# Optimization experiments

Hardware: AMD Instinct MI355X
Metric: run time of the kernel (lower is better)

## Reference

```python
import jax, jax.numpy as jnp
import numpy as np

B, N, DIM = 4, 1024, 1024
H, DH, ORDER = 16, 64, 3
MAXREL = 64
INNER = H * DH
VOCAB = 2 * MAXREL + 1
SCALE = DH ** -0.5
TOPK = int(0.25 * N)  # topk_ratio=0.25 default when top_k is None


def setup_inputs() -> dict:
    key = jax.random.key(0)
    ks = jax.random.split(key, 8)
    s = 0.02
    return {
        "x": jax.random.normal(ks[0], (B, N, DIM), jnp.float32),
        "Wqkv": jax.random.normal(ks[1], (3 * INNER, DIM), jnp.float32) * s,
        "bqkv": jnp.zeros((3 * INNER,), jnp.float32),
        "Wout": jax.random.normal(ks[2], (DIM, INNER), jnp.float32) * s,
        "bout": jnp.zeros((DIM,), jnp.float32),
        "rel_k_emb": jax.random.normal(ks[3], (VOCAB, DH), jnp.float32) * s,
        "rel_v_emb": jax.random.normal(ks[4], (VOCAB, DH), jnp.float32) * s,
        "alphas_raw": jax.random.normal(ks[5], (ORDER, H), jnp.float32) * 0.5,
    }


def reference(x, Wqkv, bqkv, Wout, bout, rel_k_emb, rel_v_emb, alphas_raw):
    b, n, _ = x.shape
    qkv = x @ Wqkv.T + bqkv  # [b, n, 3*inner]
    q, k, v = jnp.split(qkv, 3, axis=-1)
    to_heads = lambda t: t.reshape(b, n, H, DH).transpose(0, 2, 1, 3)  # b h n d
    q, k, v = to_heads(q), to_heads(k), to_heads(v)

    scores = jnp.einsum('bhid,bhjd->bhij', q, k) * SCALE

    # relative position bias on keys
    coords = jnp.arange(n)
    dist = jnp.clip(coords[:, None] - coords[None, :], -MAXREL, MAXREL) + MAXREL  # [n, n]
    rel_k = rel_k_emb[dist]  # [n, n, d]
    scores = scores + jnp.einsum('bhid,ijd->bhij', q, rel_k)

    # top-k thresholding per query row
    top_vals = jax.lax.top_k(scores, TOPK)[0]
    threshold = top_vals[..., -1:]
    scores = jnp.where(scores < threshold, -jnp.inf, scores)

    attn = jax.nn.softmax(scores, axis=-1)  # [b, h, n, n]

    rel_v = rel_v_emb[dist]  # [n, n, d]
    alphas = jax.nn.sigmoid(alphas_raw)  # [order, h]

    # monomial-basis polynomial filter: res = sum_i alpha_i * A^(i+1) V (+ relV term at i=0)
    res = jnp.zeros_like(v)
    v_curr = v
    for i in range(ORDER):
        a_v = jnp.einsum('bhij,bhjd->bhid', attn, v_curr)
        if i == 0:
            a_v = a_v + jnp.einsum('bhij,ijd->bhid', attn, rel_v)
        v_curr = a_v
        res = res + alphas[i][None, :, None, None] * v_curr

    out = res.transpose(0, 2, 1, 3).reshape(b, n, INNER)
    return out @ Wout.T + bout
```

## Files before the change

### kernel.cpp

```cpp
#include <hip/hip_runtime.h>

typedef unsigned short u16;
typedef unsigned int   u32;
typedef unsigned long long u64;
typedef __bf16 bf16x8 __attribute__((ext_vector_type(8)));
typedef float  floatx4 __attribute__((ext_vector_type(4)));

#define DEV static __device__ __forceinline__

DEV u16 f2bf(float f){ u32 x = __float_as_uint(f); return (u16)((x + 0x7fffu + ((x>>16)&1u)) >> 16); }
DEV float bf2f(u16 h){ return __uint_as_float(((u32)h)<<16); }
DEV u32 cvt_pk_bf16(float a, float b){ u32 r; asm("v_cvt_pk_bf16_f32 %0, %1, %2" : "=v"(r) : "v"(a), "v"(b)); return r; }

DEV void load_lds16(const u16* g, u16* l){
  __builtin_amdgcn_global_load_lds((const __attribute__((address_space(1))) u32*)g,
                                   (__attribute__((address_space(3))) u32*)l, 16, 0, 0);
}

DEV void barrier_fenced(){
  asm volatile("" ::: "memory");
  __builtin_amdgcn_sched_barrier(0);
  __builtin_amdgcn_s_barrier();
  __builtin_amdgcn_sched_barrier(0);
  asm volatile("" ::: "memory");
}

DEV u32 unswz64(u32 p){
  u32 r0 = ((p>>6) ^ (p>>8)) & 1u;
  u32 b4 = ((p>>4) & 1u) ^ r0;
  u32 b5 = ((p>>5) ^ (p>>7)) & 1u;
  return (p & ~0x70u) | (b4<<4) | (b5<<5) | (r0<<6);
}
DEV bf16x8 ldfrag(const u16* base, int row, int lane){
  u32 off = ((u32)row<<6) + (((u32)lane>>4)<<4);
  off ^= (u32)(row&7)<<4;
  return *(const bf16x8*)((const char*)base + off);
}

template<int BM, int BN>
__global__ __launch_bounds__(512, 4) void gemm8(
    const u16* __restrict__ A, const u16* __restrict__ Bm, float* __restrict__ C,
    const float* __restrict__ bias, int K, int lda, int ldb, int ldc, int ncmax)
{
  constexpr int MT = (BM/2)/16;
  constexpr int NT = (BN/4)/16;
  __shared__ u16 As[BM*32];
  __shared__ u16 Bs[BN*32];

  const int tid = threadIdx.x, wid = tid>>6, lane = tid&63;
  const int m0 = blockIdx.y * BM, n0 = blockIdx.x * BN;

  const u32 g = unswz64((u32)tid*16);
  const int srow = g>>6, schunk = (g&63)>>1;
  const u16* ga0 = A  + (long long)(m0 + srow)*lda + schunk;
  const u16* gb0 = Bm + (long long)(n0 + srow)*ldb + schunk;

  u16* lA = As + (wid<<9);
  u16* lB = Bs + (wid<<9);

  const int wm = wid>>2, wn = wid&3;
  const int lr = lane&15, lq = lane>>4;

  floatx4 acc[MT][NT] = {};

  for (int k = 0; k < K; k += 32) {
    __syncthreads();
    if (BM == 128 || wid < 4) load_lds16(ga0 + k, lA);
    load_lds16(gb0 + k, lB);
    __syncthreads();
    bf16x8 af[MT];
#pragma unroll
    for (int mt=0; mt<MT; ++mt)
      af[mt] = ldfrag(As, wm*(BM/2) + mt*16 + lr, lane);
#pragma unroll
    for (int nt=0; nt<NT; ++nt) {
      bf16x8 bfr = ldfrag(Bs, wn*(BN/4) + nt*16 + lr, lane);
#pragma unroll
      for (int mt=0; mt<MT; ++mt)
        acc[mt][nt] = __builtin_amdgcn_mfma_f32_16x16x32_bf16(af[mt], bfr, acc[mt][nt], 0, 0, 0);
    }
  }

#pragma unroll
  for (int nt=0; nt<NT; ++nt) {
    const int col = n0 + wn*(BN/4) + nt*16 + lr;
    if (col < ncmax) {
      const float bv = bias ? bias[col] : 0.f;
#pragma unroll
      for (int mt=0; mt<MT; ++mt) {
#pragma unroll
        for (int r=0; r<4; ++r) {
          const int row = m0 + wm*(BM/2) + mt*16 + lq*4 + r;
          C[(long long)row*ldc + col] = acc[mt][nt][r] + bv;
        }
      }
    }
  }
}

__global__ __launch_bounds__(512, 4) void av8(
    const u16* __restrict__ P,
    const u16* __restrict__ V,
    u16* __restrict__ vout,
    float* __restrict__ resb,
    const float* __restrict__ araw, int K, int order, int accum, int wv)
{
  __shared__ u16 smem[32768];
  const int tid = threadIdx.x, wid = tid>>6, lane = tid&63;
  const int L = blockIdx.x;
  const int z  = (L & 7) + ((L >> 7) << 3);
  const int m0 = ((L >> 3) & 15) * 64;
  const int lr = lane&15, lq = lane>>4;

  const int sw = wid & 3;
  const u32 g = unswz64((u32)(sw*1024 + lane*16));
  const int srow = g>>6, schunk = (g&63)>>1;
  const u16* gsrc = (wid < 4)
      ? P + (long long)z*1212416 + (long long)(m0 + srow)*1184 + schunk
      : V + (long long)z*75776   + (long long)srow*1184 + schunk;
  const int bsel = (wid < 4) ? 0 : 2048;
  u16* ldst0 = smem + bsel + (sw<<9);

  const int wm = wid>>2, wn = wid&3;
  const int wm32 = wm*32, wn16 = wn*16;
  const int nk = K >> 5;

  auto stage = [&](int p){ load_lds16(gsrc + (p<<5), ldst0 + ((p&7)<<12)); };

  floatx4 acc[2] = {};

#define AV_STEP(CC, VC) do { \
    asm volatile("s_waitcnt vmcnt(" VC ")" ::: "memory"); \
    barrier_fenced(); \
    const u16* Asc = smem + ((u32)(CC)<<12); \
    const u16* Bsc = Asc + 2048; \
    bf16x8 bfr = ldfrag(Bsc, wn16 + lr, lane); \
    bf16x8 af0 = ldfrag(Asc, wm32 + lr, lane); \
    bf16x8 af1 = ldfrag(Asc, wm32 + 16 + lr, lane); \
    acc[0] = __builtin_amdgcn_mfma_f32_16x16x32_bf16(af0, bfr, acc[0], 0, 0, 0); \
    acc[1] = __builtin_amdgcn_mfma_f32_16x16x32_bf16(af1, bfr, acc[1], 0, 0, 0); \
    barrier_fenced(); \
  } while(0)

#pragma unroll
  for (int p = 0; p < 8; ++p) stage(p);

  for (int s = 0; s < nk - 8; ++s){
    AV_STEP(s & 7, "7");
    stage(s + 8);
  }
  AV_STEP((nk-8) & 7, "7");
  AV_STEP((nk-7) & 7, "6");
  AV_STEP((nk-6) & 7, "5");
  AV_STEP((nk-5) & 7, "4");
  AV_STEP((nk-4) & 7, "3");
  AV_STEP((nk-3) & 7, "2");
  AV_STEP((nk-2) & 7, "1");
  AV_STEP((nk-1) & 7, "0");
#undef AV_STEP

  const int h = z & 15;
  const float alpha = 1.f/(1.f + __expf(-araw[order*16 + h]));
  float* rb = resb + (long long)z * 65536;
  const int d = wn16 + lr;
  __syncthreads();
#pragma unroll
  for (int mt=0; mt<2; ++mt){
#pragma unroll
    for (int r=0; r<4; ++r){
      const int row = wm32 + mt*16 + lq*4 + r;
      const float v = acc[mt][r];
      const long long ri = (long long)(m0+row)*64 + d;
      rb[ri] = accum ? (rb[ri] + alpha*v) : (alpha*v);
      smem[d*136 + row] = f2bf(v);
    }
  }
  __syncthreads();
  if (wv){
    const int dd = tid>>3, cc = (tid&7)*8;
    u16* vp = vout + (long long)z*75776 + (long long)dd*1184 + m0 + cc;
    const u16* sp = smem + dd*136 + cc;
    uint4 uu;
    uu.x = sp[0] | ((u32)sp[1]<<16);
    uu.y = sp[2] | ((u32)sp[3]<<16);
    uu.z = sp[4] | ((u32)sp[5]<<16);
    uu.w = sp[6] | ((u32)sp[7]<<16);
    *(uint4*)(vp) = uu;
  }
}

__global__ __launch_bounds__(1024, 8) void score_topk(
    const u16* __restrict__ qF,
    const u16* __restrict__ kxF,
    u16* __restrict__ P)
{
  constexpr int SROW = 1156;
  __shared__ float sm[16*SROW];
  const int tid = threadIdx.x, wid = tid>>6, lane = tid&63;
  const int L = blockIdx.x;
  const int z  = (L & 7) + ((L >> 9) << 3);
  const int mt = (L >> 3) & 63;
  const int m0 = mt*16;
  const int lr = lane&15, lq = lane>>4;

  const u16* Aq = qF + (((long long)z*64 + mt)*6*64 + lane)*8;
  const u16* Bq = kxF + ((long long)z*80*6*64 + lane)*8;

  bf16x8 af[6];
#pragma unroll
  for (int kc=0;kc<6;++kc) af[kc] = *(const bf16x8*)(Aq + kc*512);

  const int base = wid*5;
  {
    floatx4 acc[5];
#pragma unroll
    for (int t=0;t<5;++t) acc[t] = floatx4{0.f,0.f,0.f,0.f};
#pragma unroll
    for (int t=0;t<5;++t){
      if (base + t < 73){
        const u16* bp = Bq + (long long)(base+t)*3072;
        bf16x8 b0 = *(const bf16x8*)(bp);
        bf16x8 b1 = *(const bf16x8*)(bp + 512);
        bf16x8 b2 = *(const bf16x8*)(bp + 1024);
        bf16x8 b3 = *(const bf16x8*)(bp + 1536);
        bf16x8 b4 = *(const bf16x8*)(bp + 2048);
        bf16x8 b5 = *(const bf16x8*)(bp + 2560);
        acc[t] = __builtin_amdgcn_mfma_f32_16x16x32_bf16(af[0], b0, acc[t], 0, 0, 0);
        acc[t] = __builtin_amdgcn_mfma_f32_16x16x32_bf16(af[1], b1, acc[t], 0, 0, 0);
        acc[t] = __builtin_amdgcn_mfma_f32_16x16x32_bf16(af[2], b2, acc[t], 0, 0, 0);
        acc[t] = __builtin_amdgcn_mfma_f32_16x16x32_bf16(af[3], b3, acc[t], 0, 0, 0);
        acc[t] = __builtin_amdgcn_mfma_f32_16x16x32_bf16(af[4], b4, acc[t], 0, 0, 0);
        acc[t] = __builtin_amdgcn_mfma_f32_16x16x32_bf16(af[5], b5, acc[t], 0, 0, 0);
      }
    }
#pragma unroll
    for (int t=0;t<5;++t){
      if (base + t < 73){
        const int col = (base+t)*16 + lr;
        if (col < 1153){
#pragma unroll
          for (int r=0;r<4;++r) sm[(lq*4+r)*SROW + col] = acc[t][r];
        }
      }
    }
  }
  __syncthreads();

  {
    const int row = wid;
    const int i = m0 + row;
    float* R = sm + row*SROW;

    float v[16];
#pragma unroll
    for (int x=0;x<8;++x){
      float2 f = *(const float2*)(R + x*128 + lane*2);
      v[2*x] = f.x; v[2*x+1] = f.y;
    }
#pragma unroll
    for (int x=0;x<16;++x){
      const int j = (x>>1)*128 + lane*2 + (x&1);
      int dl = i - j; dl = dl > 64 ? 64 : (dl < -64 ? -64 : dl);
      v[x] += R[1024 + dl + 64];
    }
    u32 u[16];
#pragma unroll
    for (int x=0;x<16;++x){
      u32 bb = __float_as_uint(v[x]);
      u[x] = bb ^ ((u32)((int)bb >> 31) | 0x80000000u);
    }
    u32 thr = 0;
#pragma unroll 1
    for (int bit=31; bit>=0; --bit){
      const u32 cand = thr | (1u<<bit);
      int c = 0;
#pragma unroll
      for (int x=0;x<16;++x) c += __popcll(__ballot(u[x] >= cand));
      if (c == 256){
        u32 mn = 0xFFFFFFFFu;
#pragma unroll
        for (int x=0;x<16;++x) if (u[x] >= cand && u[x] < mn) mn = u[x];
        for (int o=32;o;o>>=1){ u32 t = __shfl_xor(mn, o); mn = t < mn ? t : mn; }
        thr = mn;
        break;
      }
      if (c > 256) thr = cand;
    }
    float m = -3.0e38f;
#pragma unroll
    for (int x=0;x<16;++x) m = fmaxf(m, v[x]);
    for (int o=32;o;o>>=1) m = fmaxf(m, __shfl_xor(m, o));
    float e[16]; float Z = 0.f;
#pragma unroll
    for (int x=0;x<16;++x){
      e[x] = (u[x] >= thr) ? __expf(v[x]-m) : 0.f;
      Z += e[x];
    }
    for (int o=32;o;o>>=1) Z += __shfl_xor(Z, o);
    const float rz = 1.f / Z;

    u16* Pr = P + ((long long)z*1024 + i)*1184;
    u32* Pr32 = (u32*)Pr;
    float s0 = 0.f, s1 = 0.f;
#pragma unroll
    for (int x=0;x<8;++x){
      const float p0 = e[2*x]*rz, p1 = e[2*x+1]*rz;
      *(float2*)(R + x*128 + lane*2) = float2{p0, p1};
      Pr32[x*64 + lane] = cvt_pk_bf16(p0, p1);
      const int j0 = x*128 + lane*2;
      if (j0     >= i+64) s0 += p0;
      if (j0     <= i-64) s1 += p0;
      if (j0 + 1 >= i+64) s0 += p1;
      if (j0 + 1 <= i-64) s1 += p1;
    }
    for (int o=32;o;o>>=1){ s0 += __shfl_xor(s0,o); s1 += __shfl_xor(s1,o); }
    {
      const int t = lane + 1;
      const int j = i + 64 - t;
      const float wv = (j>=0 && j<1024) ? R[j] : 0.f;
      Pr[1024 + t] = f2bf(wv);
      if (lane < 63){
        const int t2 = lane + 65;
        const int j2 = i + 64 - t2;
        const float wv2 = (j2>=0 && j2<1024) ? R[j2] : 0.f;
        Pr[1024 + t2] = f2bf(wv2);
      }
      if (lane == 0){ Pr[1024] = f2bf(s0); Pr[1152] = f2bf(s1); }
      if (lane >= 33) Pr[1120 + lane] = 0;
    }
  }
}

__global__ __launch_bounds__(256) void planeize(const float* __restrict__ src, u16* __restrict__ dst,
                                                int total, int modeB){
  int idx = blockIdx.x*256 + threadIdx.x;
  if (idx >= total) return;
  int c = idx & 1023, r = idx >> 10;
  float v = src[idx];
  u16 hi = f2bf(v); u16 lo = f2bf(v - bf2f(hi));
  u16* d = dst + (long long)r*3072 + c;
  if (modeB){ d[0]=hi; d[1024]=hi; d[2048]=lo; }
  else      { d[0]=hi; d[1024]=lo; d[2048]=hi; }
}

__global__ __launch_bounds__(256) void build_qk(const float* __restrict__ qkv,
                                                u16* __restrict__ qF, u16* __restrict__ kxF){
  int idx = blockIdx.x*256 + threadIdx.x;
  int d = idx & 63, n = (idx>>6) & 1023, bh = idx >> 16;
  int b = bh >> 4, h = bh & 15;
  long long src = (long long)(b*1024 + n)*3072 + h*64 + d;
  float qv = qkv[src];
  float kv = qkv[src + 1024] * 0.125f;
  u16 qhi=f2bf(qv), qlo=f2bf(qv - bf2f(qhi));
  u16 khi=f2bf(kv), klo=f2bf(kv - bf2f(khi));
  const int lane = (n&15) + (((d&31)>>3)<<4);
  const int elem = d&7, kc0 = d>>5;
  u16* q = qF + ((((long long)bh*64 + (n>>4))*6*64) + lane)*8 + elem;
  q[(kc0+0)*512] = qhi; q[(kc0+2)*512] = qlo; q[(kc0+4)*512] = qhi;
  u16* kx = kxF + ((((long long)bh*80 + (n>>4))*6*64) + lane)*8 + elem;
  kx[(kc0+0)*512] = khi; kx[(kc0+2)*512] = khi; kx[(kc0+4)*512] = klo;
}

__global__ __launch_bounds__(256) void build_kxrel(const float* __restrict__ relk, u16* __restrict__ kxF){
  int idx = blockIdx.x*256 + threadIdx.x;
  int d = idx & 63, t = (idx>>6) & 255, bh = idx >> 14;
  u16 hi=0, lo=0;
  if (t < 129){ float v = relk[t*64 + d]; hi = f2bf(v); lo = f2bf(v - bf2f(hi)); }
  const int nrow = 1024 + t;
  const int lane = (t&15) + (((d&31)>>3)<<4);
  const int elem = d&7, kc0 = d>>5;
  u16* kx = kxF + ((((long long)bh*80 + (nrow>>4))*6*64) + lane)*8 + elem;
  kx[(kc0+0)*512] = hi; kx[(kc0+2)*512] = hi; kx[(kc0+4)*512] = lo;
}

__global__ __launch_bounds__(256) void build_vT(const float* __restrict__ qkv, u16* __restrict__ vA){
  __shared__ float tb[64][65];
  int bh = blockIdx.x >> 4, ntile = blockIdx.x & 15;
  int b = bh >> 4, h = bh & 15;
  int tid = threadIdx.x;
  int nl = tid >> 2, dc = (tid & 3)*16;
  const float* sp = qkv + (long long)(b*1024 + ntile*64 + nl)*3072 + 2048 + h*64 + dc;
#pragma unroll
  for (int j=0;j<16;j+=4){
    float4 f = *(const float4*)(sp + j);
    tb[dc+j+0][nl]=f.x; tb[dc+j+1][nl]=f.y; tb[dc+j+2][nl]=f.z; tb[dc+j+3][nl]=f.w;
  }
  __syncthreads();
  int d = tid >> 2, nc = (tid & 3)*16;
  u16* dp = vA + ((long long)bh*64 + d)*1184 + ntile*64 + nc;
#pragma unroll
  for (int j=0;j<16;j+=8){
    u16 a0=f2bf(tb[d][nc+j+0]), a1=f2bf(tb[d][nc+j+1]), a2=f2bf(tb[d][nc+j+2]), a3=f2bf(tb[d][nc+j+3]);
    u16 a4=f2bf(tb[d][nc+j+4]), a5=f2bf(tb[d][nc+j+5]), a6=f2bf(tb[d][nc+j+6]), a7=f2bf(tb[d][nc+j+7]);
    uint4 uu; uu.x=a0|((u32)a1<<16); uu.y=a2|((u32)a3<<16); uu.z=a4|((u32)a5<<16); uu.w=a6|((u32)a7<<16);
    *(uint4*)(dp + j) = uu;
  }
}

__global__ __launch_bounds__(256) void build_vText(const float* __restrict__ relv, u16* __restrict__ vA){
  int idx = blockIdx.x*256 + threadIdx.x;
  int t = idx % 160; int rest = idx / 160; int d = rest & 63; int bh = rest >> 6;
  u16 hv = 0;
  if (t < 129) hv = f2bf(relv[t*64 + d]);
  vA[((long long)bh*64 + d)*1184 + 1024 + t] = hv;
}

__global__ __launch_bounds__(256) void build_resS(const float* __restrict__ res, u16* __restrict__ resS){
  int idx = blockIdx.x*256 + threadIdx.x;
  int d = idx & 63, n = (idx>>6) & 1023, bh = idx >> 16;
  int b = bh >> 4, h = bh & 15;
  float v = res[idx];
  u16 hi = f2bf(v), lo = f2bf(v - bf2f(hi));
  u16* p = resS + (long long)(b*1024 + n)*3072 + h*64 + d;
  p[0]=hi; p[1024]=lo; p[2048]=hi;
}

extern "C" void kernel_launch(void* const* d_in, const int* in_sizes, int n_in,
                              void* d_out, int out_size, void* d_ws, size_t ws_size,
                              hipStream_t stream) {
  const float* x    = (const float*)d_in[0];
  const float* Wqkv = (const float*)d_in[1];
  const float* bqkv = (const float*)d_in[2];
  const float* Wout = (const float*)d_in[3];
  const float* bout = (const float*)d_in[4];
  const float* relk = (const float*)d_in[5];
  const float* relv = (const float*)d_in[6];
  const float* araw = (const float*)d_in[7];
  float* out = (float*)d_out;

  char* w = (char*)d_ws;
  size_t off = 0;
  auto take = [&](size_t bytes)->char*{ char* p = w + off; off += (bytes + 255) & ~(size_t)255; return p; };

  char* regionA = take(94371840);
  u16*   xS    = (u16*)  (regionA);
  u16*   wqS   = (u16*)  (regionA + 25165824);
  float* qkv32 = (float*)(regionA + 44040192);
  u16*   Ph    = (u16*)  (regionA);
  u16*   resS  = (u16*)  (regionA);
  u16*   woS   = (u16*)  (regionA + 25165824);
  u16*   qF    = (u16*)take(25165824);
  u16*   kxF   = (u16*)take(31457280);
  u16*   vA    = (u16*)take(9699328);
  u16*   vB    = (u16*)take(9699328);
  float* res   = (float*)take(16777216);
  (void)ws_size; (void)in_sizes; (void)n_in; (void)out_size;

  planeize<<<16384,256,0,stream>>>(x,    xS,  4194304, 0);
  planeize<<<12288,256,0,stream>>>(Wqkv, wqS, 3145728, 1);
  gemm8<128,128><<<dim3(16,32,1),512,0,stream>>>(xS, wqS, qkv32, bqkv,
      3072, 3072, 3072, 3072, 2048);
  gemm8<128,128><<<dim3(8,32,1),512,0,stream>>>(xS, wqS + (long long)2048*3072,
      qkv32 + 2048, bqkv + 2048, 1024, 3072, 3072, 3072, 1024);
  build_qk   <<<16384,256,0,stream>>>(qkv32, qF, kxF);
  build_kxrel<<<4096, 256,0,stream>>>(relk, kxF);
  build_vT   <<<1024, 256,0,stream>>>(qkv32, vA);
  build_vText<<<2560, 256,0,stream>>>(relv, vA);

  for (int half = 0; half < 2; ++half) {
    const long long zo = (long long)half * 32;
    score_topk<<<2048,1024,0,stream>>>(qF + zo*196608, kxF + zo*245760, Ph);
    av8<<<512,512,0,stream>>>(Ph, vA + zo*75776, vB + zo*75776, res + zo*65536,
        araw, 1184, 0, 0, 1);
    av8<<<512,512,0,stream>>>(Ph, vB + zo*75776, vA + zo*75776, res + zo*65536,
        araw, 1024, 1, 1, 1);
    av8<<<512,512,0,stream>>>(Ph, vA + zo*75776, vB + zo*75776, res + zo*65536,
        araw, 1024, 2, 1, 0);
  }

  build_resS<<<16384,256,0,stream>>>(res, resS);
  planeize  <<<4096, 256,0,stream>>>(Wout, woS, 1048576, 1);
  gemm8<64,128><<<dim3(8,64,1),512,0,stream>>>(resS, woS, out, bout,
      3072, 3072, 3072, 1024, 1024);
}
```

Baseline: 556.5 us.

## Add four-stage async LDS pipeline to gemm8 K loop

Replaces the single-buffered K loop in the bf16 GEMM with a four-deep ring of LDS buffers. Global-to-LDS loads are issued four tiles ahead and tracked with explicit vmcnt waits, so memory latency overlaps MFMA work instead of stalling at each barrier. This multiplies LDS use by four, which may reduce occupancy under launch_bounds(512,4). It also assumes K is at least 128 and relies on hand-counted vmcnt values.

```diff
diff --git a/kernel.cpp b/kernel.cpp
--- a/kernel.cpp
+++ b/kernel.cpp
@@ -44,8 +44,10 @@
 {
   constexpr int MT = (BM/2)/16;
   constexpr int NT = (BN/4)/16;
-  __shared__ u16 As[BM*32];
-  __shared__ u16 Bs[BN*32];
+  constexpr int AU = BM*32;
+  constexpr int BU = BN*32;
+  constexpr int STRIDE = AU + BU;
+  __shared__ u16 smem[4*STRIDE];
 
   const int tid = threadIdx.x, wid = tid>>6, lane = tid&63;
   const int m0 = blockIdx.y * BM, n0 = blockIdx.x * BN;
@@ -55,31 +57,52 @@
   const u16* ga0 = A  + (long long)(m0 + srow)*lda + schunk;
   const u16* gb0 = Bm + (long long)(n0 + srow)*ldb + schunk;
 
-  u16* lA = As + (wid<<9);
-  u16* lB = Bs + (wid<<9);
+  u16* lA0 = smem + (wid<<9);
+  u16* lB0 = smem + AU + (wid<<9);
 
   const int wm = wid>>2, wn = wid&3;
   const int lr = lane&15, lq = lane>>4;
 
+  auto stage = [&](int s){
+    const int c = s & 3;
+    if (BM == 128 || wid < 4) load_lds16(ga0 + (s<<5), lA0 + c*STRIDE);
+    load_lds16(gb0 + (s<<5), lB0 + c*STRIDE);
+  };
+
   floatx4 acc[MT][NT] = {};
-
-  for (int k = 0; k < K; k += 32) {
-    __syncthreads();
-    if (BM == 128 || wid < 4) load_lds16(ga0 + k, lA);
-    load_lds16(gb0 + k, lB);
-    __syncthreads();
-    bf16x8 af[MT];
-#pragma unroll
-    for (int mt=0; mt<MT; ++mt)
-      af[mt] = ldfrag(As, wm*(BM/2) + mt*16 + lr, lane);
-#pragma unroll
-    for (int nt=0; nt<NT; ++nt) {
-      bf16x8 bfr = ldfrag(Bs, wn*(BN/4) + nt*16 + lr, lane);
-#pragma unroll
-      for (int mt=0; mt<MT; ++mt)
-        acc[mt][nt] = __builtin_amdgcn_mfma_f32_16x16x32_bf16(af[mt], bfr, acc[mt][nt], 0, 0, 0);
-    }
-  }
+  const int nk = K >> 5;
+
+#define G_STEP(CC, VA, VB) do { \
+    if (BM == 128 || wid < 4) asm volatile("s_waitcnt vmcnt(" VA ")" ::: "memory"); \
+    else                      asm volatile("s_waitcnt vmcnt(" VB ")" ::: "memory"); \
+    barrier_fenced(); \
+    const u16* Asc = smem + (u32)(CC)*STRIDE; \
+    const u16* Bsc = Asc + AU; \
+    bf16x8 af[MT]; \
+    _Pragma("unroll") \
+    for (int mt=0; mt<MT; ++mt) af[mt] = ldfrag(Asc, wm*(BM/2) + mt*16 + lr, lane); \
+    _Pragma("unroll") \
+    for (int nt=0; nt<NT; ++nt) { \
+      bf16x8 bfr = ldfrag(Bsc, wn*(BN/4) + nt*16 + lr, lane); \
+      _Pragma("unroll") \
+      for (int mt=0; mt<MT; ++mt) \
+        acc[mt][nt] = __builtin_amdgcn_mfma_f32_16x16x32_bf16(af[mt], bfr, acc[mt][nt], 0, 0, 0); \
+    } \
+    barrier_fenced(); \
+  } while(0)
+
+#pragma unroll
+  for (int p = 0; p < 4; ++p) stage(p);
+
+  for (int s = 0; s < nk - 4; ++s){
+    G_STEP(s & 3, "6", "3");
+    stage(s + 4);
+  }
+  G_STEP((nk-4) & 3, "6", "3");
+  G_STEP((nk-3) & 3, "4", "2");
+  G_STEP((nk-2) & 3, "2", "1");
+  G_STEP((nk-1) & 3, "0", "0");
+#undef G_STEP
 
 #pragma unroll
   for (int nt=0; nt<NT; ++nt) {
```

New measurement: 538.1 us. -3.3%, faster.
